# Optimization experiments

Hardware: AMD Instinct MI355X
Metric: run time of the kernel (lower is better)

## Reference

```python
import jax, jax.numpy as jnp
import numpy as np

B, S, D, H = 2, 2048, 1024, 16
HD = D // H  # head_dim = 64


def setup_inputs() -> dict:
    key = jax.random.key(0)
    ks = jax.random.split(key, 5)
    scale = 1.0 / np.sqrt(D)
    return {
        "x": jax.random.normal(ks[0], (B, S, D), dtype=jnp.float32),
        "w_q": jax.random.normal(ks[1], (D, D), dtype=jnp.float32) * scale,
        "b_q": jnp.zeros((D,), dtype=jnp.float32),
        "w_k": jax.random.normal(ks[2], (D, D), dtype=jnp.float32) * scale,
        "b_k": jnp.zeros((D,), dtype=jnp.float32),
        "w_v": jax.random.normal(ks[3], (D, D), dtype=jnp.float32) * scale,
        "b_v": jnp.zeros((D,), dtype=jnp.float32),
        "w_out": jax.random.normal(ks[4], (D, D), dtype=jnp.float32) * scale,
        "b_out": jnp.zeros((D,), dtype=jnp.float32),
    }


def reference(x, w_q, b_q, w_k, b_k, w_v, b_v, w_out, b_out):
    # Linear projections (torch Linear: x @ W.T + b)
    q = x @ w_q.T + b_q
    k = x @ w_k.T + b_k
    v = x @ w_v.T + b_v
    # split heads: [B, S, D] -> [B, H, S, HD]
    split = lambda t: t.reshape(B, S, H, HD).transpose(0, 2, 1, 3)
    q, k, v = split(q), split(k), split(v)
    # scaled dot-product attention with causal (tril) mask
    scores = jnp.einsum("bhqd,bhkd->bhqk", q, k) / jnp.sqrt(jnp.float32(HD))
    causal = jnp.tril(jnp.ones((S, S), dtype=bool))  # mask from causal_masking_function
    scores = jnp.where(causal, scores, jnp.float32(-1e9))
    probs = jax.nn.softmax(scores, axis=-1)
    # dropout(0.1) is identity in eval mode
    out = jnp.einsum("bhqk,bhkd->bhqd", probs, v)
    out = out.transpose(0, 2, 1, 3).reshape(B, S, D)
    return out @ w_out.T + b_out
```

## Files before the change

### kernel.cpp

```cpp
#include <hip/hip_runtime.h>

typedef __attribute__((ext_vector_type(8))) short bf16x8;
typedef __attribute__((ext_vector_type(4))) float f32x4;

__device__ __forceinline__ unsigned short f2b(float f) {
    unsigned u = __builtin_bit_cast(unsigned, f);
    u += 0x7fffu + ((u >> 16) & 1u);
    return (unsigned short)(u >> 16);
}

#define GLD_LDS(gp, lp) __builtin_amdgcn_global_load_lds( \
    (const __attribute__((address_space(1))) void*)(gp),  \
    (__attribute__((address_space(3))) void*)(lp), 16, 0, 0)

#define MFMA16(a, b, cacc) __builtin_amdgcn_mfma_f32_16x16x32_bf16(a, b, cacc, 0, 0, 0)

#define QSCL 0.18033688011112042f

__global__ __launch_bounds__(256) void cvt_all(const float* __restrict__ x,
        const float* __restrict__ w0, const float* __restrict__ w1,
        const float* __restrict__ w2, const float* __restrict__ w3,
        short* xb, short* o0, short* o1, short* o2, short* o3) {
    int i = blockIdx.x * 256 + threadIdx.x;
    const float* in; short* out; int off; float scl = 1.0f;
    if (i < (1 << 20)) { in = x; out = xb; off = i; }
    else {
        int j = (i - (1 << 20)) >> 18;
        off = (i - (1 << 20)) & ((1 << 18) - 1);
        switch (j) {
            case 0: in = w0; out = o0; scl = QSCL; break;
            case 1: in = w1; out = o1; break;
            case 2: in = w2; out = o2; break;
            default: in = w3; out = o3; break;
        }
    }
    float4 v = reinterpret_cast<const float4*>(in)[off];
    short4 o;
    o.x = (short)f2b(v.x * scl); o.y = (short)f2b(v.y * scl);
    o.z = (short)f2b(v.z * scl); o.w = (short)f2b(v.w * scl);
    reinterpret_cast<short4*>(out)[off] = o;
}

__global__ __launch_bounds__(256) void qkv_gemm(const short* __restrict__ A,
        const short* __restrict__ Wq, const short* __restrict__ Wk, const short* __restrict__ Wv,
        const float* __restrict__ bq, const float* __restrict__ bk, const float* __restrict__ bv,
        short* __restrict__ Oq, short* __restrict__ Ok, short* __restrict__ Ovt) {
    constexpr int Kd = 1024, N = 1024, S = 2048;
    __shared__ short As[128 * 64];
    __shared__ short Bs[128 * 64];
    const int mat = blockIdx.x >> 3;
    const int n0 = (blockIdx.x & 7) * 128, m0 = blockIdx.y * 128;
    const short* Bm = (mat == 0) ? Wq : (mat == 1 ? Wk : Wv);
    const float* bias = (mat == 0) ? bq : (mat == 1 ? bk : bv);
    const float bscl = (mat == 0) ? QSCL : 1.0f;
    const int t = threadIdx.x;
    const int w = t >> 6, lane = t & 63;
    const int wm = w >> 1, wn = w & 1;
    const int c = lane & 15, g = lane >> 4;

    f32x4 acc[4][4] = {};

    for (int k0 = 0; k0 < Kd; k0 += 64) {
#pragma unroll
        for (int cc = 0; cc < 4; ++cc) {
            int e = (cc * 256 + t) * 8;
            int row = e >> 6, col = e & 63;
            GLD_LDS(A + (size_t)(m0 + row) * Kd + k0 + col, As + e);
            GLD_LDS(Bm + (size_t)(n0 + row) * Kd + k0 + col, Bs + e);
        }
        __syncthreads();
#pragma unroll
        for (int kk = 0; kk < 2; ++kk) {
            bf16x8 af[4], bfr[4];
#pragma unroll
            for (int mi = 0; mi < 4; ++mi)
                af[mi] = *(const bf16x8*)(As + (wm * 64 + mi * 16 + c) * 64 + kk * 32 + g * 8);
#pragma unroll
            for (int ni = 0; ni < 4; ++ni)
                bfr[ni] = *(const bf16x8*)(Bs + (wn * 64 + ni * 16 + c) * 64 + kk * 32 + g * 8);
#pragma unroll
            for (int mi = 0; mi < 4; ++mi)
#pragma unroll
                for (int ni = 0; ni < 4; ++ni)
                    acc[mi][ni] = MFMA16(af[mi], bfr[ni], acc[mi][ni]);
        }
        __syncthreads();
    }

    if (mat < 2) {
        short* Cb = (mat == 0) ? Oq : Ok;
#pragma unroll
        for (int mi = 0; mi < 4; ++mi)
#pragma unroll
            for (int ni = 0; ni < 4; ++ni) {
                int col = n0 + wn * 64 + ni * 16 + c;
                float bvv = bias[col] * bscl;
#pragma unroll
                for (int r = 0; r < 4; ++r) {
                    int row = m0 + wm * 64 + mi * 16 + g * 4 + r;
                    Cb[(size_t)row * N + col] = (short)f2b(acc[mi][ni][r] + bvv);
                }
            }
    } else {
#pragma unroll
        for (int mi = 0; mi < 4; ++mi)
#pragma unroll
            for (int ni = 0; ni < 4; ++ni) {
                int col = n0 + wn * 64 + ni * 16 + c;
                int h = col >> 6, hd = col & 63;
                float bvv = bias[col];
                int row0 = m0 + wm * 64 + mi * 16 + g * 4;
                int b = row0 >> 11, s = row0 & 2047;
                short4 pk;
                pk.x = (short)f2b(acc[mi][ni][0] + bvv);
                pk.y = (short)f2b(acc[mi][ni][1] + bvv);
                pk.z = (short)f2b(acc[mi][ni][2] + bvv);
                pk.w = (short)f2b(acc[mi][ni][3] + bvv);
                *(short4*)(Ovt + ((size_t)((b * 16 + h) * 64 + hd)) * S + s) = pk;
            }
    }
}

__global__ __launch_bounds__(256) void out_gemm(const short* __restrict__ A,
                                                const short* __restrict__ Bm,
                                                const float* __restrict__ bias,
                                                float* __restrict__ C) {
    constexpr int Kd = 1024, N = 1024;
    __shared__ short As[64 * 64];
    __shared__ short Bs[128 * 64];
    const int n0 = blockIdx.x * 128, m0 = blockIdx.y * 64;
    const int t = threadIdx.x;
    const int w = t >> 6, lane = t & 63;
    const int wm = w >> 1, wn = w & 1;
    const int c = lane & 15, g = lane >> 4;

    f32x4 acc[2][4] = {};

    for (int k0 = 0; k0 < Kd; k0 += 64) {
#pragma unroll
        for (int cc = 0; cc < 2; ++cc) {
            int e = (cc * 256 + t) * 8;
            GLD_LDS(A + (size_t)(m0 + (e >> 6)) * Kd + k0 + (e & 63), As + e);
        }
#pragma unroll
        for (int cc = 0; cc < 4; ++cc) {
            int e = (cc * 256 + t) * 8;
            GLD_LDS(Bm + (size_t)(n0 + (e >> 6)) * Kd + k0 + (e & 63), Bs + e);
        }
        __syncthreads();
#pragma unroll
        for (int kk = 0; kk < 2; ++kk) {
            bf16x8 af[2], bfr[4];
#pragma unroll
            for (int mi = 0; mi < 2; ++mi)
                af[mi] = *(const bf16x8*)(As + (wm * 32 + mi * 16 + c) * 64 + kk * 32 + g * 8);
#pragma unroll
            for (int ni = 0; ni < 4; ++ni)
                bfr[ni] = *(const bf16x8*)(Bs + (wn * 64 + ni * 16 + c) * 64 + kk * 32 + g * 8);
#pragma unroll
            for (int mi = 0; mi < 2; ++mi)
#pragma unroll
                for (int ni = 0; ni < 4; ++ni)
                    acc[mi][ni] = MFMA16(af[mi], bfr[ni], acc[mi][ni]);
        }
        __syncthreads();
    }

#pragma unroll
    for (int mi = 0; mi < 2; ++mi)
#pragma unroll
        for (int ni = 0; ni < 4; ++ni) {
            int col = n0 + wn * 64 + ni * 16 + c;
            float bvv = bias[col];
#pragma unroll
            for (int r = 0; r < 4; ++r) {
                int row = m0 + wm * 32 + mi * 16 + g * 4 + r;
                C[(size_t)row * N + col] = acc[mi][ni][r] + bvv;
            }
        }
}

__global__ __launch_bounds__(256) void attn_kernel(const short* Q,
                                                   const short* __restrict__ Kg,
                                                   const short* __restrict__ Vt,
                                                   short* O) {
    constexpr int S = 2048, D = 1024;
    constexpr float M2 = 16.0f;
    __shared__ short Ks[64 * 64];
    __shared__ short Vs[64 * 64];
    __shared__ short Pl[4][16 * 64];
    const int id = blockIdx.x;
    const int bh = id & 31, b = bh >> 4, h = bh & 15;
    const int qtile = 31 - (id >> 5);
    const int t = threadIdx.x;
    const int w = t >> 6, lane = t & 63;
    const int c = lane & 15, g = lane >> 4;
    const int q0 = qtile * 64 + w * 16;

    const short* Qb = Q + (size_t)b * S * D + h * 64;
    const short* Kp = Kg + (size_t)b * S * D + h * 64;
    const short* Vp = Vt + (size_t)bh * 64 * S;

    bf16x8 aq0 = *(const bf16x8*)(Qb + (size_t)(q0 + c) * D + g * 8);
    bf16x8 aq1 = *(const bf16x8*)(Qb + (size_t)(q0 + c) * D + 32 + g * 8);

    f32x4 o[4] = {};
    float l_part[4] = {0.f, 0.f, 0.f, 0.f};

    const int ktmax = qtile + 1;
    for (int kt = 0; kt < ktmax; ++kt) {
        const int k0 = kt * 64;
#pragma unroll
        for (int cc = 0; cc < 2; ++cc) {
            int row = cc * 32 + (t >> 3);
            int colb = ((t & 7) * 16) ^ ((row & 7) << 4);
            GLD_LDS(Kp + (size_t)(k0 + row) * D + (colb >> 1), Ks + cc * 2048 + t * 8);
            GLD_LDS(Vp + (size_t)row * S + k0 + (colb >> 1), Vs + cc * 2048 + t * 8);
        }
        __syncthreads();

        f32x4 sc[4];
#pragma unroll
        for (int nt = 0; nt < 4; ++nt) {
            int row = nt * 16 + c;
            int sw = (row & 7) << 4;
            const char* rb = (const char*)Ks + row * 128;
            bf16x8 bk0 = *(const bf16x8*)(rb + ((g * 16) ^ sw));
            bf16x8 bk1 = *(const bf16x8*)(rb + ((64 + g * 16) ^ sw));
            f32x4 z = {};
            z = MFMA16(aq0, bk0, z);
            z = MFMA16(aq1, bk1, z);
            sc[nt] = z;
        }
        if (kt == ktmax - 1) {
#pragma unroll
            for (int nt = 0; nt < 4; ++nt)
#pragma unroll
                for (int r = 0; r < 4; ++r) {
                    int key = k0 + nt * 16 + c;
                    int qr = q0 + g * 4 + r;
                    if (key > qr) sc[nt][r] = -3e38f;
                }
        }
        char* pw = (char*)&Pl[w][0];
#pragma unroll
        for (int nt = 0; nt < 4; ++nt)
#pragma unroll
            for (int r = 0; r < 4; ++r) {
                float p = __builtin_exp2f(sc[nt][r] - M2);
                l_part[r] += p;
                int prow = g * 4 + r;
                int pb = ((nt * 16 + c) * 2) ^ ((prow & 7) << 4);
                *(short*)(pw + prow * 128 + pb) = (short)f2b(p);
            }
        asm volatile("" ::: "memory");
#pragma unroll
        for (int half = 0; half < 2; ++half) {
            bf16x8 pa = *(const bf16x8*)(pw + c * 128 + ((half * 64 + g * 16) ^ ((c & 7) << 4)));
#pragma unroll
            for (int n2 = 0; n2 < 4; ++n2) {
                int vrow = n2 * 16 + c;
                bf16x8 bv = *(const bf16x8*)((const char*)Vs + vrow * 128 +
                                             ((half * 64 + g * 16) ^ ((vrow & 7) << 4)));
                o[n2] = MFMA16(pa, bv, o[n2]);
            }
        }
        __syncthreads();
    }

#pragma unroll
    for (int d = 1; d < 16; d <<= 1)
#pragma unroll
        for (int r = 0; r < 4; ++r) l_part[r] += __shfl_xor(l_part[r], d);

    short* Ob = O + (size_t)b * S * D + h * 64;
#pragma unroll
    for (int r = 0; r < 4; ++r) {
        float inv = 1.0f / l_part[r];
        int row = q0 + g * 4 + r;
#pragma unroll
        for (int n2 = 0; n2 < 4; ++n2)
            Ob[(size_t)row * D + n2 * 16 + c] = (short)f2b(o[n2][r] * inv);
    }
}

extern "C" void kernel_launch(void* const* d_in, const int* in_sizes, int n_in,
                              void* d_out, int out_size, void* d_ws, size_t ws_size,
                              hipStream_t stream) {
    const float* x  = (const float*)d_in[0];
    const float* wq = (const float*)d_in[1];
    const float* bq = (const float*)d_in[2];
    const float* wk = (const float*)d_in[3];
    const float* bk = (const float*)d_in[4];
    const float* wv = (const float*)d_in[5];
    const float* bv = (const float*)d_in[6];
    const float* wo = (const float*)d_in[7];
    const float* bo = (const float*)d_in[8];
    float* out = (float*)d_out;

    char* ws = (char*)d_ws;
    const size_t SZ_X = (size_t)4096 * 1024 * 2;
    const size_t SZ_W = (size_t)1024 * 1024 * 2;
    short* xb  = (short*)(ws);
    short* wqb = (short*)(ws + SZ_X);
    short* wkb = (short*)(ws + SZ_X + SZ_W);
    short* wvb = (short*)(ws + SZ_X + 2 * SZ_W);
    short* wob = (short*)(ws + SZ_X + 3 * SZ_W);
    short* Qb  = (short*)(ws + SZ_X + 4 * SZ_W);
    short* Kbuf= (short*)(ws + 2 * SZ_X + 4 * SZ_W);
    short* Vtb = (short*)(ws + 3 * SZ_X + 4 * SZ_W);
    short* Ab  = Qb;

    cvt_all<<<8192, 256, 0, stream>>>(x, wq, wk, wv, wo, xb, wqb, wkb, wvb, wob);

    qkv_gemm<<<dim3(24, 32), 256, 0, stream>>>(xb, wqb, wkb, wvb, bq, bk, bv, Qb, Kbuf, Vtb);

    attn_kernel<<<1024, 256, 0, stream>>>(Qb, Kbuf, Vtb, Ab);

    out_gemm<<<dim3(8, 64), 256, 0, stream>>>(Ab, wob, bo, out);
}
```

Measured before the change: 210.5 us.

## Double-buffer GEMM LDS tiles with K=32 stages and XOR-swizzled layout

Both projection GEMMs now use two LDS buffers of 32-wide K slices. Each iteration issues global-to-LDS loads for the next slice before computing on the current one, so memory latency overlaps with MFMA work and one barrier per step is removed. The LDS layout is XOR-swizzled by row to cut bank conflicts on the fragment reads. Smaller K steps double the loop iterations and barriers per block, which adds per-step overhead.

```diff
diff --git a/kernel.cpp b/kernel.cpp
--- a/kernel.cpp
+++ b/kernel.cpp
@@ -46,8 +46,8 @@
         const float* __restrict__ bq, const float* __restrict__ bk, const float* __restrict__ bv,
         short* __restrict__ Oq, short* __restrict__ Ok, short* __restrict__ Ovt) {
     constexpr int Kd = 1024, N = 1024, S = 2048;
-    __shared__ short As[128 * 64];
-    __shared__ short Bs[128 * 64];
+    __shared__ short As[2][128 * 32];
+    __shared__ short Bs[2][128 * 32];
     const int mat = blockIdx.x >> 3;
     const int n0 = (blockIdx.x & 7) * 128, m0 = blockIdx.y * 128;
     const short* Bm = (mat == 0) ? Wq : (mat == 1 ? Wk : Wv);
@@ -60,31 +60,42 @@
 
     f32x4 acc[4][4] = {};
 
-    for (int k0 = 0; k0 < Kd; k0 += 64) {
-#pragma unroll
-        for (int cc = 0; cc < 4; ++cc) {
+    auto stage = [&](int buf, int k0) {
+#pragma unroll
+        for (int cc = 0; cc < 2; ++cc) {
             int e = (cc * 256 + t) * 8;
-            int row = e >> 6, col = e & 63;
-            GLD_LDS(A + (size_t)(m0 + row) * Kd + k0 + col, As + e);
-            GLD_LDS(Bm + (size_t)(n0 + row) * Kd + k0 + col, Bs + e);
-        }
+            int row = e >> 5;
+            int col = (e & 31) ^ (((row >> 1) & 3) << 3);
+            GLD_LDS(A + (size_t)(m0 + row) * Kd + k0 + col, &As[buf][e]);
+            GLD_LDS(Bm + (size_t)(n0 + row) * Kd + k0 + col, &Bs[buf][e]);
+        }
+    };
+
+    stage(0, 0);
+    __syncthreads();
+    int cur = 0;
+    for (int ks = 0; ks < 32; ++ks) {
+        if (ks + 1 < 32) stage(cur ^ 1, (ks + 1) * 32);
+        const short* Ab_ = As[cur];
+        const short* Bb_ = Bs[cur];
+        bf16x8 af[4], bfr[4];
+#pragma unroll
+        for (int mi = 0; mi < 4; ++mi) {
+            int ar = wm * 64 + mi * 16 + c;
+            af[mi] = *(const bf16x8*)(Ab_ + ar * 32 + ((g * 8) ^ (((ar >> 1) & 3) << 3)));
+        }
+#pragma unroll
+        for (int ni = 0; ni < 4; ++ni) {
+            int br = wn * 64 + ni * 16 + c;
+            bfr[ni] = *(const bf16x8*)(Bb_ + br * 32 + ((g * 8) ^ (((br >> 1) & 3) << 3)));
+        }
+#pragma unroll
+        for (int mi = 0; mi < 4; ++mi)
+#pragma unroll
+            for (int ni = 0; ni < 4; ++ni)
+                acc[mi][ni] = MFMA16(af[mi], bfr[ni], acc[mi][ni]);
         __syncthreads();
-#pragma unroll
-        for (int kk = 0; kk < 2; ++kk) {
-            bf16x8 af[4], bfr[4];
-#pragma unroll
-            for (int mi = 0; mi < 4; ++mi)
-                af[mi] = *(const bf16x8*)(As + (wm * 64 + mi * 16 + c) * 64 + kk * 32 + g * 8);
-#pragma unroll
-            for (int ni = 0; ni < 4; ++ni)
-                bfr[ni] = *(const bf16x8*)(Bs + (wn * 64 + ni * 16 + c) * 64 + kk * 32 + g * 8);
-#pragma unroll
-            for (int mi = 0; mi < 4; ++mi)
-#pragma unroll
-                for (int ni = 0; ni < 4; ++ni)
-                    acc[mi][ni] = MFMA16(af[mi], bfr[ni], acc[mi][ni]);
-        }
-        __syncthreads();
+        cur ^= 1;
     }
 
     if (mat < 2) {
@@ -126,8 +137,8 @@
                                                 const float* __restrict__ bias,
                                                 float* __restrict__ C) {
     constexpr int Kd = 1024, N = 1024;
-    __shared__ short As[64 * 64];
-    __shared__ short Bs[128 * 64];
+    __shared__ short As[2][64 * 32];
+    __shared__ short Bs[2][128 * 32];
     const int n0 = blockIdx.x * 128, m0 = blockIdx.y * 64;
     const int t = threadIdx.x;
     const int w = t >> 6, lane = t & 63;
@@ -136,34 +147,47 @@
 
     f32x4 acc[2][4] = {};
 
-    for (int k0 = 0; k0 < Kd; k0 += 64) {
+    auto stage = [&](int buf, int k0) {
+        {
+            int e = t * 8;
+            int row = e >> 5;
+            int col = (e & 31) ^ (((row >> 1) & 3) << 3);
+            GLD_LDS(A + (size_t)(m0 + row) * Kd + k0 + col, &As[buf][e]);
+        }
 #pragma unroll
         for (int cc = 0; cc < 2; ++cc) {
             int e = (cc * 256 + t) * 8;
-            GLD_LDS(A + (size_t)(m0 + (e >> 6)) * Kd + k0 + (e & 63), As + e);
-        }
-#pragma unroll
-        for (int cc = 0; cc < 4; ++cc) {
-            int e = (cc * 256 + t) * 8;
-            GLD_LDS(Bm + (size_t)(n0 + (e >> 6)) * Kd + k0 + (e & 63), Bs + e);
-        }
+            int row = e >> 5;
+            int col = (e & 31) ^ (((row >> 1) & 3) << 3);
+            GLD_LDS(Bm + (size_t)(n0 + row) * Kd + k0 + col, &Bs[buf][e]);
+        }
+    };
+
+    stage(0, 0);
+    __syncthreads();
+    int cur = 0;
+    for (int ks = 0; ks < 32; ++ks) {
+        if (ks + 1 < 32) stage(cur ^ 1, (ks + 1) * 32);
+        const short* Ab_ = As[cur];
+        const short* Bb_ = Bs[cur];
+        bf16x8 af[2], bfr[4];
+#pragma unroll
+        for (int mi = 0; mi < 2; ++mi) {
+            int ar = wm * 32 + mi * 16 + c;
+            af[mi] = *(const bf16x8*)(Ab_ + ar * 32 + ((g * 8) ^ (((ar >> 1) & 3) << 3)));
+        }
+#pragma unroll
+        for (int ni = 0; ni < 4; ++ni) {
+            int br = wn * 64 + ni * 16 + c;
+            bfr[ni] = *(const bf16x8*)(Bb_ + br * 32 + ((g * 8) ^ (((br >> 1) & 3) << 3)));
+        }
+#pragma unroll
+        for (int mi = 0; mi < 2; ++mi)
+#pragma unroll
+            for (int ni = 0; ni < 4; ++ni)
+                acc[mi][ni] = MFMA16(af[mi], bfr[ni], acc[mi][ni]);
         __syncthreads();
-#pragma unroll
-        for (int kk = 0; kk < 2; ++kk) {
-            bf16x8 af[2], bfr[4];
-#pragma unroll
-            for (int mi = 0; mi < 2; ++mi)
-                af[mi] = *(const bf16x8*)(As + (wm * 32 + mi * 16 + c) * 64 + kk * 32 + g * 8);
-#pragma unroll
-            for (int ni = 0; ni < 4; ++ni)
-                bfr[ni] = *(const bf16x8*)(Bs + (wn * 64 + ni * 16 + c) * 64 + kk * 32 + g * 8);
-#pragma unroll
-            for (int mi = 0; mi < 2; ++mi)
-#pragma unroll
-                for (int ni = 0; ni < 4; ++ni)
-                    acc[mi][ni] = MFMA16(af[mi], bfr[ni], acc[mi][ni]);
-        }
-        __syncthreads();
+        cur ^= 1;
     }
 
 #pragma unroll
```

Measured after the change: 209.3 us. Within noise of the previous version (-0.6%).

## Drop LDS staging in projection GEMMs; load MFMA fragments directly from global

Applied to the files above, without the earlier changes.

Both the QKV and output-projection GEMMs stop staging tiles in shared memory through global_load_lds and barriers. Each wave now reads its bf16 fragments straight from global memory into registers and computes a 64x64 tile. Blocks shrink to two waves covering 128x64. This removes LDS traffic and __syncthreads stalls, but loses cross-wave reuse in LDS, so more global and L2 traffic goes through strided 16-byte loads.

```diff
diff --git a/kernel.cpp b/kernel.cpp
--- a/kernel.cpp
+++ b/kernel.cpp
@@ -41,50 +41,39 @@
     reinterpret_cast<short4*>(out)[off] = o;
 }
 
-__global__ __launch_bounds__(256) void qkv_gemm(const short* __restrict__ A,
+__global__ __launch_bounds__(128) void qkv_gemm(const short* __restrict__ A,
         const short* __restrict__ Wq, const short* __restrict__ Wk, const short* __restrict__ Wv,
         const float* __restrict__ bq, const float* __restrict__ bk, const float* __restrict__ bv,
         short* __restrict__ Oq, short* __restrict__ Ok, short* __restrict__ Ovt) {
     constexpr int Kd = 1024, N = 1024, S = 2048;
-    __shared__ short As[128 * 64];
-    __shared__ short Bs[128 * 64];
-    const int mat = blockIdx.x >> 3;
-    const int n0 = (blockIdx.x & 7) * 128, m0 = blockIdx.y * 128;
+    const int mat = blockIdx.z;
     const short* Bm = (mat == 0) ? Wq : (mat == 1 ? Wk : Wv);
     const float* bias = (mat == 0) ? bq : (mat == 1 ? bk : bv);
     const float bscl = (mat == 0) ? QSCL : 1.0f;
-    const int t = threadIdx.x;
-    const int w = t >> 6, lane = t & 63;
-    const int wm = w >> 1, wn = w & 1;
+    const int n0 = blockIdx.x * 64;
+    const int w = threadIdx.x >> 6, lane = threadIdx.x & 63;
+    const int m0 = blockIdx.y * 128 + w * 64;
     const int c = lane & 15, g = lane >> 4;
 
+    const short* pA = A + (size_t)(m0 + c) * Kd + g * 8;
+    const short* pB = Bm + (size_t)(n0 + c) * Kd + g * 8;
+
     f32x4 acc[4][4] = {};
 
-    for (int k0 = 0; k0 < Kd; k0 += 64) {
-#pragma unroll
-        for (int cc = 0; cc < 4; ++cc) {
-            int e = (cc * 256 + t) * 8;
-            int row = e >> 6, col = e & 63;
-            GLD_LDS(A + (size_t)(m0 + row) * Kd + k0 + col, As + e);
-            GLD_LDS(Bm + (size_t)(n0 + row) * Kd + k0 + col, Bs + e);
-        }
-        __syncthreads();
-#pragma unroll
-        for (int kk = 0; kk < 2; ++kk) {
-            bf16x8 af[4], bfr[4];
-#pragma unroll
-            for (int mi = 0; mi < 4; ++mi)
-                af[mi] = *(const bf16x8*)(As + (wm * 64 + mi * 16 + c) * 64 + kk * 32 + g * 8);
+#pragma unroll 2
+    for (int kk = 0; kk < 32; ++kk) {
+        bf16x8 af[4], bfr[4];
+#pragma unroll
+        for (int mi = 0; mi < 4; ++mi)
+            af[mi] = *(const bf16x8*)(pA + mi * 16 * Kd + kk * 32);
+#pragma unroll
+        for (int ni = 0; ni < 4; ++ni)
+            bfr[ni] = *(const bf16x8*)(pB + ni * 16 * Kd + kk * 32);
+#pragma unroll
+        for (int mi = 0; mi < 4; ++mi)
 #pragma unroll
             for (int ni = 0; ni < 4; ++ni)
-                bfr[ni] = *(const bf16x8*)(Bs + (wn * 64 + ni * 16 + c) * 64 + kk * 32 + g * 8);
-#pragma unroll
-            for (int mi = 0; mi < 4; ++mi)
-#pragma unroll
-                for (int ni = 0; ni < 4; ++ni)
-                    acc[mi][ni] = MFMA16(af[mi], bfr[ni], acc[mi][ni]);
-        }
-        __syncthreads();
+                acc[mi][ni] = MFMA16(af[mi], bfr[ni], acc[mi][ni]);
     }
 
     if (mat < 2) {
@@ -93,11 +82,11 @@
         for (int mi = 0; mi < 4; ++mi)
 #pragma unroll
             for (int ni = 0; ni < 4; ++ni) {
-                int col = n0 + wn * 64 + ni * 16 + c;
+                int col = n0 + ni * 16 + c;
                 float bvv = bias[col] * bscl;
 #pragma unroll
                 for (int r = 0; r < 4; ++r) {
-                    int row = m0 + wm * 64 + mi * 16 + g * 4 + r;
+                    int row = m0 + mi * 16 + g * 4 + r;
                     Cb[(size_t)row * N + col] = (short)f2b(acc[mi][ni][r] + bvv);
                 }
             }
@@ -106,10 +95,10 @@
         for (int mi = 0; mi < 4; ++mi)
 #pragma unroll
             for (int ni = 0; ni < 4; ++ni) {
-                int col = n0 + wn * 64 + ni * 16 + c;
+                int col = n0 + ni * 16 + c;
                 int h = col >> 6, hd = col & 63;
                 float bvv = bias[col];
-                int row0 = m0 + wm * 64 + mi * 16 + g * 4;
+                int row0 = m0 + mi * 16 + g * 4;
                 int b = row0 >> 11, s = row0 & 2047;
                 short4 pk;
                 pk.x = (short)f2b(acc[mi][ni][0] + bvv);
@@ -121,60 +110,46 @@
     }
 }
 
-__global__ __launch_bounds__(256) void out_gemm(const short* __restrict__ A,
+__global__ __launch_bounds__(128) void out_gemm(const short* __restrict__ A,
                                                 const short* __restrict__ Bm,
                                                 const float* __restrict__ bias,
                                                 float* __restrict__ C) {
     constexpr int Kd = 1024, N = 1024;
-    __shared__ short As[64 * 64];
-    __shared__ short Bs[128 * 64];
-    const int n0 = blockIdx.x * 128, m0 = blockIdx.y * 64;
-    const int t = threadIdx.x;
-    const int w = t >> 6, lane = t & 63;
-    const int wm = w >> 1, wn = w & 1;
+    const int n0 = blockIdx.x * 64;
+    const int w = threadIdx.x >> 6, lane = threadIdx.x & 63;
+    const int m0 = blockIdx.y * 128 + w * 64;
     const int c = lane & 15, g = lane >> 4;
 
-    f32x4 acc[2][4] = {};
-
-    for (int k0 = 0; k0 < Kd; k0 += 64) {
-#pragma unroll
-        for (int cc = 0; cc < 2; ++cc) {
-            int e = (cc * 256 + t) * 8;
-            GLD_LDS(A + (size_t)(m0 + (e >> 6)) * Kd + k0 + (e & 63), As + e);
-        }
-#pragma unroll
-        for (int cc = 0; cc < 4; ++cc) {
-            int e = (cc * 256 + t) * 8;
-            GLD_LDS(Bm + (size_t)(n0 + (e >> 6)) * Kd + k0 + (e & 63), Bs + e);
-        }
-        __syncthreads();
-#pragma unroll
-        for (int kk = 0; kk < 2; ++kk) {
-            bf16x8 af[2], bfr[4];
-#pragma unroll
-            for (int mi = 0; mi < 2; ++mi)
-                af[mi] = *(const bf16x8*)(As + (wm * 32 + mi * 16 + c) * 64 + kk * 32 + g * 8);
+    const short* pA = A + (size_t)(m0 + c) * Kd + g * 8;
+    const short* pB = Bm + (size_t)(n0 + c) * Kd + g * 8;
+
+    f32x4 acc[4][4] = {};
+
+#pragma unroll 2
+    for (int kk = 0; kk < 32; ++kk) {
+        bf16x8 af[4], bfr[4];
+#pragma unroll
+        for (int mi = 0; mi < 4; ++mi)
+            af[mi] = *(const bf16x8*)(pA + mi * 16 * Kd + kk * 32);
+#pragma unroll
+        for (int ni = 0; ni < 4; ++ni)
+            bfr[ni] = *(const bf16x8*)(pB + ni * 16 * Kd + kk * 32);
+#pragma unroll
+        for (int mi = 0; mi < 4; ++mi)
 #pragma unroll
             for (int ni = 0; ni < 4; ++ni)
-                bfr[ni] = *(const bf16x8*)(Bs + (wn * 64 + ni * 16 + c) * 64 + kk * 32 + g * 8);
-#pragma unroll
-            for (int mi = 0; mi < 2; ++mi)
-#pragma unroll
-                for (int ni = 0; ni < 4; ++ni)
-                    acc[mi][ni] = MFMA16(af[mi], bfr[ni], acc[mi][ni]);
-        }
-        __syncthreads();
-    }
-
-#pragma unroll
-    for (int mi = 0; mi < 2; ++mi)
+                acc[mi][ni] = MFMA16(af[mi], bfr[ni], acc[mi][ni]);
+    }
+
+#pragma unroll
+    for (int mi = 0; mi < 4; ++mi)
 #pragma unroll
         for (int ni = 0; ni < 4; ++ni) {
-            int col = n0 + wn * 64 + ni * 16 + c;
+            int col = n0 + ni * 16 + c;
             float bvv = bias[col];
 #pragma unroll
             for (int r = 0; r < 4; ++r) {
-                int row = m0 + wm * 32 + mi * 16 + g * 4 + r;
+                int row = m0 + mi * 16 + g * 4 + r;
                 C[(size_t)row * N + col] = acc[mi][ni][r] + bvv;
             }
         }
@@ -313,9 +288,9 @@
 
     cvt_all<<<8192, 256, 0, stream>>>(x, wq, wk, wv, wo, xb, wqb, wkb, wvb, wob);
 
-    qkv_gemm<<<dim3(24, 32), 256, 0, stream>>>(xb, wqb, wkb, wvb, bq, bk, bv, Qb, Kbuf, Vtb);
+    qkv_gemm<<<dim3(16, 32, 3), 128, 0, stream>>>(xb, wqb, wkb, wvb, bq, bk, bv, Qb, Kbuf, Vtb);
 
     attn_kernel<<<1024, 256, 0, stream>>>(Qb, Kbuf, Vtb, Ab);
 
-    out_gemm<<<dim3(8, 64), 256, 0, stream>>>(Ab, wob, bo, out);
-}
+    out_gemm<<<dim3(16, 32), 128, 0, stream>>>(Ab, wob, bo, out);
+}
```

Result: slower. 291.3 us (+38.4%).
